# Performance work log

Measured on AMD Instinct MI355X. Metric: run time of the kernel, lower is better.

## Reference

```python
import jax, jax.numpy as jnp
import numpy as np

BN_EPS = 1e-5


def _bn(x, gamma, beta):
    # BatchNorm2d in training mode: batch statistics over (B, T, V) per channel.
    mean = jnp.mean(x, axis=(0, 2, 3), keepdims=True)
    var = jnp.var(x, axis=(0, 2, 3), keepdims=True)
    inv = jax.lax.rsqrt(var + BN_EPS)
    g = gamma[None, :, None, None]
    b = beta[None, :, None, None]
    return (x - mean) * inv * g + b


def setup_inputs() -> dict:
    key = jax.random.key(0)
    ks = jax.random.split(key, 8)
    B, Cin, Cout, T, V = 32, 64, 128, 300, 25
    x = jax.random.normal(ks[0], (B, Cin, T, V), dtype=jnp.float32)
    A_hat = jax.random.uniform(ks[1], (V, V), dtype=jnp.float32) / V  # row-normalized-ish adjacency
    # spatial 1x1 conv weight/bias
    w_sp = jax.random.normal(ks[2], (Cout, Cin), dtype=jnp.float32) * (1.0 / np.sqrt(Cin))
    b_sp = jnp.zeros((Cout,), dtype=jnp.float32)
    g_sp = jnp.ones((Cout,), dtype=jnp.float32)
    be_sp = jnp.zeros((Cout,), dtype=jnp.float32)
    # temporal conv (9,1) weight/bias, same channels
    w_t = jax.random.normal(ks[3], (Cout, Cout, 9, 1), dtype=jnp.float32) * (1.0 / np.sqrt(Cout * 9))
    b_t = jnp.zeros((Cout,), dtype=jnp.float32)
    g_t = jnp.ones((Cout,), dtype=jnp.float32)
    be_t = jnp.zeros((Cout,), dtype=jnp.float32)
    # residual 1x1 conv + BN (in_channels != out_channels)
    w_r = jax.random.normal(ks[4], (Cout, Cin), dtype=jnp.float32) * (1.0 / np.sqrt(Cin))
    b_r = jnp.zeros((Cout,), dtype=jnp.float32)
    g_r = jnp.ones((Cout,), dtype=jnp.float32)
    be_r = jnp.zeros((Cout,), dtype=jnp.float32)
    return {
        "x": x, "A_hat": A_hat,
        "w_sp": w_sp, "b_sp": b_sp, "g_sp": g_sp, "be_sp": be_sp,
        "w_t": w_t, "b_t": b_t, "g_t": g_t, "be_t": be_t,
        "w_r": w_r, "b_r": b_r, "g_r": g_r, "be_r": be_r,
    }


def reference(x, A_hat, w_sp, b_sp, g_sp, be_sp, w_t, b_t, g_t, be_t, w_r, b_r, g_r, be_r):
    # residual branch: 1x1 conv + BN
    res = jnp.einsum('oc,bctv->botv', w_r, x) + b_r[None, :, None, None]
    res = _bn(res, g_r, be_r)
    # spatial graph conv: A_hat @ x over node dim, then 1x1 conv
    h = jnp.einsum('vw,bctw->bctv', A_hat, x)
    h = jnp.einsum('oc,bctv->botv', w_sp, h) + b_sp[None, :, None, None]
    h = jax.nn.relu(_bn(h, g_sp, be_sp))
    # temporal conv (9,1) with padding (4,0), then BN
    h = jax.lax.conv_general_dilated(
        h, w_t, window_strides=(1, 1), padding=((4, 4), (0, 0)),
        dimension_numbers=('NCHW', 'OIHW', 'NCHW'))
    h = h + b_t[None, :, None, None]
    h = _bn(h, g_t, be_t)
    return jax.nn.relu(h + res)
```

## Files before the change

### kernel.cpp

```cpp
#include <hip/hip_runtime.h>

constexpr int B    = 32;
constexpr int CIN  = 64;
constexpr int COUT = 128;
constexpr int T    = 300;
constexpr int V    = 25;
constexpr int TV   = T * V;
constexpr long long NPC   = (long long)B * TV;
constexpr long long TOTAL = (long long)B * COUT * TV;

typedef short          bf16x8 __attribute__((ext_vector_type(8)));
typedef float          f32x4  __attribute__((ext_vector_type(4)));
typedef unsigned short us8    __attribute__((ext_vector_type(8)));
typedef unsigned short us4    __attribute__((ext_vector_type(4)));

static __device__ __forceinline__ unsigned short f2bf(float f) {
  union { float f; unsigned u; } x; x.f = f;
  unsigned r = x.u + 0x7FFFu + ((x.u >> 16) & 1u);
  return (unsigned short)(r >> 16);
}
static __device__ __forceinline__ float bf2f(unsigned short u) {
  union { unsigned u; float f; } x; x.u = ((unsigned)u) << 16;
  return x.f;
}
static __device__ __forceinline__ unsigned cvtpk(float a, float b) {
  unsigned r;
  asm("v_cvt_pk_bf16_f32 %0, %1, %2" : "=v"(r) : "v"(a), "v"(b));
  return r;
}

static __device__ __forceinline__ int xoff(int pos, int c) {
  return pos * 64 + ((((c >> 3)) ^ (pos & 7)) << 3) + (c & 7);
}
static __device__ __forceinline__ int soff(int c, int pw) {
  return c * 128 + ((((pw >> 3)) ^ (c & 7)) << 3) + (pw & 7);
}

__global__ __launch_bounds__(256) void kPrep(
    const float* __restrict__ w_t, const float* __restrict__ w_r,
    const float* __restrict__ w_sp, const float* __restrict__ A_hat,
    unsigned short* __restrict__ wb2, unsigned short* __restrict__ wrs2,
    unsigned short* __restrict__ bdt)
{
  int i = blockIdx.x * 256 + threadIdx.x;
  if (i < 147456) {
    int c = i & 127, ok = i >> 7;
    int k = ok % 9, o = ok / 9;
    int idx = ((k * 16 + (c >> 3)) * 128 + o) * 8 + (c & 7);
    wb2[idx] = f2bf(w_t[(o * COUT + c) * 9 + k]);
  } else if (i < 147456 + 16384) {
    int j = i - 147456;
    int c = j & 63, row = j >> 6;
    float v = (row < COUT) ? w_r[row * CIN + c] : w_sp[(row - COUT) * CIN + c];
    wrs2[((c >> 3) * 256 + row) * 8 + (c & 7)] = f2bf(v);
  } else {
    int j = i - 147456 - 16384;
    int pv = j >> 7, pw = j & 127;
    float v = 0.f;
    if (pv < 100 && pw < 100 && (pv / 25) == (pw / 25))
      v = A_hat[(pv % 25) * 25 + (pw % 25)];
    bdt[j] = f2bf(v);
  }
}

__global__ __launch_bounds__(256, 2) void kA6(
    const float* __restrict__ x, const unsigned short* __restrict__ bdt,
    const unsigned short* __restrict__ wrs2,
    unsigned short* __restrict__ resb, unsigned short* __restrict__ h,
    float2* __restrict__ part_rs)
{
  __shared__ unsigned short xs[64 * 128];
  __shared__ unsigned short xsp[112 * 64];
  unsigned short* axsp = xs;

  const int tid  = threadIdx.x;
  const int lane = tid & 63;
  const int wave = tid >> 6;
  const int b    = blockIdx.y;
  const int p0   = blockIdx.x * 100;
  const int grp  = lane >> 4;
  const int l15  = lane & 15;

  for (int u = tid; u < 16 * 128; u += 256) {
    int pos = u & 127, c4 = u >> 7;
    int c0 = c4 * 4;
    float v0 = 0.f, v1 = 0.f, v2 = 0.f, v3 = 0.f;
    if (pos < 100) {
      const float* xp = &x[(b * CIN + c0) * TV + p0 + pos];
      v0 = xp[0]; v1 = xp[TV]; v2 = xp[2 * TV]; v3 = xp[3 * TV];
    }
    unsigned short b0 = f2bf(v0), b1 = f2bf(v1), b2 = f2bf(v2), b3 = f2bf(v3);
    xs[soff(c0,     pos)] = b0;
    xs[soff(c0 + 1, pos)] = b1;
    xs[soff(c0 + 2, pos)] = b2;
    xs[soff(c0 + 3, pos)] = b3;
    if (pos < 112) {
      us4 pk = {b0, b1, b2, b3};
      *(us4*)&xsp[xoff(pos, c0)] = pk;
    }
  }
  __syncthreads();

  bf16x8 xf[4];
#pragma unroll
  for (int ks = 0; ks < 4; ++ks)
    xf[ks] = *(const bf16x8*)&xs[soff(wave * 16 + l15, ks * 32 + grp * 8)];
  __syncthreads();

  {
    f32x4 macc[7];
#pragma unroll
    for (int ni = 0; ni < 7; ++ni) macc[ni] = (f32x4)0.f;
    const int kst[7] = {0, 0, 0, 0, 1, 2, 2};
    const int kcn[7] = {1, 2, 2, 3, 3, 2, 2};
#pragma unroll
    for (int ni = 0; ni < 7; ++ni) {
      for (int kk = 0; kk < kcn[ni]; ++kk) {
        int ks = kst[ni] + kk;
        bf16x8 gf = *(const bf16x8*)&bdt[(ni * 16 + l15) * 128 + ks * 32 + grp * 8];
        macc[ni] = __builtin_amdgcn_mfma_f32_16x16x32_bf16(xf[ks], gf, macc[ni], 0, 0, 0);
      }
    }
#pragma unroll
    for (int ni = 0; ni < 7; ++ni) {
#pragma unroll
      for (int r = 0; r < 4; ++r)
        axsp[xoff(ni * 16 + l15, wave * 16 + grp * 4 + r)] = f2bf(macc[ni][r]);
    }
  }
  __syncthreads();

  const unsigned short* bsrc = (wave < 2) ? xsp : axsp;
  f32x4 acc[4][7];
#pragma unroll
  for (int m = 0; m < 4; ++m)
#pragma unroll
    for (int n = 0; n < 7; ++n) acc[m][n] = (f32x4)0.f;

#pragma unroll
  for (int ks = 0; ks < 2; ++ks) {
    bf16x8 af[4], bfr[7];
#pragma unroll
    for (int mi = 0; mi < 4; ++mi) {
      int row = wave * 64 + mi * 16 + l15;
      af[mi] = *(const bf16x8*)&wrs2[((ks * 4 + grp) * 256 + row) * 8];
    }
#pragma unroll
    for (int ni = 0; ni < 7; ++ni)
      bfr[ni] = *(const bf16x8*)&bsrc[xoff(ni * 16 + l15, ks * 32 + grp * 8)];
#pragma unroll
    for (int mi = 0; mi < 4; ++mi)
#pragma unroll
      for (int ni = 0; ni < 7; ++ni)
        acc[mi][ni] = __builtin_amdgcn_mfma_f32_16x16x32_bf16(
            af[mi], bfr[ni], acc[mi][ni], 0, 0, 0);
  }

  if (wave < 2) {
#pragma unroll
    for (int mi = 0; mi < 4; ++mi) {
#pragma unroll
      for (int ni = 0; ni < 7; ++ni) {
        int pos = ni * 16 + l15;
        if (pos < 100) {
#pragma unroll
          for (int r = 0; r < 4; ++r) {
            int c = wave * 64 + mi * 16 + grp * 4 + r;
            resb[((long long)(b * COUT + c)) * TV + p0 + pos] = f2bf(acc[mi][ni][r]);
          }
        }
      }
    }
  } else {
#pragma unroll
    for (int mi = 0; mi < 4; ++mi) {
      int o0 = (wave - 2) * 64 + mi * 16 + grp * 4;
#pragma unroll
      for (int ni = 0; ni < 7; ++ni) {
        int pos = ni * 16 + l15;
        if (pos < 100) {
          uint2 w;
          w.x = cvtpk(acc[mi][ni][0], acc[mi][ni][1]);
          w.y = cvtpk(acc[mi][ni][2], acc[mi][ni][3]);
          *(uint2*)&h[((long long)(b * TV + p0 + pos)) * COUT + o0] = w;
        }
      }
    }
  }

  {
    float sv[16], qv[16];
#pragma unroll
    for (int mi = 0; mi < 4; ++mi)
#pragma unroll
      for (int r = 0; r < 4; ++r) {
        float s = 0.f, q = 0.f;
#pragma unroll
        for (int ni = 0; ni < 7; ++ni) {
          float v = (ni < 6 || l15 < 4) ? acc[mi][ni][r] : 0.f;
          s += v; q += v * v;
        }
        sv[mi * 4 + r] = s; qv[mi * 4 + r] = q;
      }
#pragma unroll
    for (int bm = 1; bm < 16; bm <<= 1) {
      const bool up = (l15 & bm) != 0;
#pragma unroll
      for (int i = 0; i < 16; i += 2 * bm) {
        const int j = i + bm;
        float ssend = up ? sv[i] : sv[j];
        float qsend = up ? qv[i] : qv[j];
        float sgot = __shfl_xor(ssend, bm);
        float qgot = __shfl_xor(qsend, bm);
        sv[i] = (up ? sv[j] : sv[i]) + sgot;
        qv[i] = (up ? qv[j] : qv[i]) + qgot;
      }
    }
    int slot = ((l15 >> 2) * 16) + grp * 4 + (l15 & 3);
    float2* pw = &part_rs[(((long long)(blockIdx.y * 75 + blockIdx.x)) * 4 + wave) * 64];
    pw[slot] = make_float2(sv[0], qv[0]);
  }
}

__global__ __launch_bounds__(256) void kC2v2(
    const float2* __restrict__ part_rs,
    const float* __restrict__ g_r,  const float* __restrict__ be_r,
    const float* __restrict__ g_sp, const float* __restrict__ be_sp,
    float* __restrict__ scales)
{
  __shared__ float rs[256], rq[256];
  const int row = blockIdx.x;
  const int wave = row >> 6, local = row & 63;
  const int tid = threadIdx.x;
  float s = 0.f, q = 0.f;
  for (int bid = tid; bid < 2400; bid += 256) {
    float2 v = part_rs[((long long)bid * 4 + wave) * 64 + local];
    s += v.x; q += v.y;
  }
  rs[tid] = s; rq[tid] = q;
  __syncthreads();
  for (int st = 128; st > 0; st >>= 1) {
    if (tid < st) { rs[tid] += rs[tid + st]; rq[tid] += rq[tid + st]; }
    __syncthreads();
  }
  if (tid == 0) {
    const float n = (float)NPC;
    float m = rs[0] / n, var = rq[0] / n - m * m;
    float iv = rsqrtf(var + 1e-5f);
    if (row < 128) {
      float sc = g_r[row] * iv;
      scales[row] = sc; scales[128 + row] = be_r[row] - m * sc;
    } else {
      int c = row - 128;
      float sc = g_sp[c] * iv;
      scales[256 + c] = sc; scales[384 + c] = be_sp[c] - m * sc;
    }
  }
}

constexpr int NP    = 256;
constexpr int HALO  = 100;
constexpr int STAGE = NP + 2 * HALO;

__global__ __launch_bounds__(512, 2) void kE7d(
    const unsigned short* __restrict__ h, const unsigned short* __restrict__ wb2,
    const float* __restrict__ scales, unsigned short* __restrict__ cvb,
    float2* __restrict__ part_t)
{
  __shared__ unsigned short hs[STAGE * 64];
  const int tid  = threadIdx.x;
  const int lane = tid & 63;
  const int wave = tid >> 6;
  const int wm   = wave >> 2, wn = wave & 3;
  const int b    = blockIdx.y;
  const int p0   = blockIdx.x * NP;
  const int grp  = lane >> 4;
  const int l15  = lane & 15;
  const int slot = tid & 7;

  f32x4 acc[4][4];
#pragma unroll
  for (int m = 0; m < 4; ++m)
#pragma unroll
    for (int n = 0; n < 4; ++n) acc[m][n] = (f32x4)0.f;

  for (int cc = 0; cc < 2; ++cc) {
    if (cc) __syncthreads();
    const int c0 = cc * 64;
    float sc[8], sh[8];
#pragma unroll
    for (int e = 0; e < 8; ++e) {
      sc[e] = scales[256 + c0 + slot * 8 + e];
      sh[e] = scales[384 + c0 + slot * 8 + e];
    }
    for (int i = tid; i < STAGE * 8; i += 512) {
      int pos = i >> 3;
      int pg = p0 - HALO + pos;
      uint4 w = {0u, 0u, 0u, 0u};
      if (pg >= 0 && pg < TV) {
        us8 v = *(const us8*)&h[((long long)b * TV + pg) * COUT + c0 + slot * 8];
        float f[8];
#pragma unroll
        for (int e = 0; e < 8; ++e)
          f[e] = fmaxf(bf2f(v[e]) * sc[e] + sh[e], 0.f);
        w.x = cvtpk(f[0], f[1]);
        w.y = cvtpk(f[2], f[3]);
        w.z = cvtpk(f[4], f[5]);
        w.w = cvtpk(f[6], f[7]);
      }
      int si = (pos << 6) + ((slot ^ (pos & 7)) << 3);
      *(uint4*)&hs[si] = w;
    }
    __syncthreads();

    __builtin_amdgcn_s_setprio(1);
    for (int k = 0; k < 9; ++k) {
      const int plb = HALO + wn * 64 + 25 * (k - 4) + l15;
#pragma unroll
      for (int ks = 0; ks < 2; ++ks) {
        bf16x8 af[4], bfr[4];
#pragma unroll
        for (int mi = 0; mi < 4; ++mi) {
          int o = wm * 64 + mi * 16 + l15;
          af[mi] = *(const bf16x8*)&wb2[((k * 16 + cc * 8 + ks * 4 + grp) * 128 + o) * 8];
        }
#pragma unroll
        for (int ni = 0; ni < 4; ++ni) {
          int pl = plb + ni * 16;
          int si = (pl << 6) + (((ks * 4 + grp) ^ (pl & 7)) << 3);
          bfr[ni] = *(const bf16x8*)&hs[si];
        }
#pragma unroll
        for (int mi = 0; mi < 4; ++mi)
#pragma unroll
          for (int ni = 0; ni < 4; ++ni)
            acc[mi][ni] = __builtin_amdgcn_mfma_f32_16x16x32_bf16(
                af[mi], bfr[ni], acc[mi][ni], 0, 0, 0);
      }
    }
    __builtin_amdgcn_s_setprio(0);
  }

#pragma unroll
  for (int mi = 0; mi < 4; ++mi) {
#pragma unroll
    for (int ni = 0; ni < 4; ++ni) {
      int pos = p0 + wn * 64 + ni * 16 + l15;
      if (pos < TV) {
#pragma unroll
        for (int r = 0; r < 4; ++r) {
          int o = wm * 64 + mi * 16 + grp * 4 + r;
          cvb[((long long)(b * COUT + o)) * TV + pos] = f2bf(acc[mi][ni][r]);
        }
      }
    }
  }

  {
    float sv[16], qv[16];
#pragma unroll
    for (int mi = 0; mi < 4; ++mi)
#pragma unroll
      for (int r = 0; r < 4; ++r) {
        float s = 0.f, q = 0.f;
#pragma unroll
        for (int ni = 0; ni < 4; ++ni) {
          int pos = p0 + wn * 64 + ni * 16 + l15;
          float v = (pos < TV) ? acc[mi][ni][r] : 0.f;
          s += v; q += v * v;
        }
        sv[mi * 4 + r] = s; qv[mi * 4 + r] = q;
      }
#pragma unroll
    for (int bm = 1; bm < 16; bm <<= 1) {
      const bool up = (l15 & bm) != 0;
#pragma unroll
      for (int i = 0; i < 16; i += 2 * bm) {
        const int j = i + bm;
        float ssend = up ? sv[i] : sv[j];
        float qsend = up ? qv[i] : qv[j];
        float sgot = __shfl_xor(ssend, bm);
        float qgot = __shfl_xor(qsend, bm);
        sv[i] = (up ? sv[j] : sv[i]) + sgot;
        qv[i] = (up ? qv[j] : qv[i]) + qgot;
      }
    }
    int slt = ((l15 >> 2) * 16) + grp * 4 + (l15 & 3);
    float2* pw = &part_t[(((long long)(blockIdx.y * 30 + blockIdx.x)) * 8 + wave) * 64];
    pw[slt] = make_float2(sv[0], qv[0]);
  }
}

__global__ __launch_bounds__(256) void kG2(
    const float2* __restrict__ part_t,
    const float* __restrict__ g_t, const float* __restrict__ be_t,
    float* __restrict__ scales)
{
  __shared__ float rs[256], rq[256];
  const int c = blockIdx.x;
  const int wm = c >> 6, local = c & 63;
  const int tid = threadIdx.x;
  const int NB = 30 * 32;
  float s = 0.f, q = 0.f;
  for (int p = tid; p < NB * 4; p += 256) {
    int bid = p >> 2, wn = p & 3;
    float2 v = part_t[((long long)bid * 8 + (wm * 4 + wn)) * 64 + local];
    s += v.x; q += v.y;
  }
  rs[tid] = s; rq[tid] = q;
  __syncthreads();
  for (int st = 128; st > 0; st >>= 1) {
    if (tid < st) { rs[tid] += rs[tid + st]; rq[tid] += rq[tid + st]; }
    __syncthreads();
  }
  if (tid == 0) {
    const float n = (float)NPC;
    float m = rs[0] / n, var = rq[0] / n - m * m;
    float sc = g_t[c] * rsqrtf(var + 1e-5f);
    scales[512 + c] = sc;
    scales[640 + c] = be_t[c] - m * sc;
  }
}

__global__ __launch_bounds__(256) void kH(
    const unsigned short* __restrict__ cvb, const unsigned short* __restrict__ resb,
    const float* __restrict__ scales, float* __restrict__ out)
{
  const int plane = blockIdx.x;
  const int c = plane & 127;
  const float sct = scales[512 + c], sht = scales[640 + c];
  const float scr = scales[c],       shr = scales[128 + c];
  const us4* cp = (const us4*)&cvb[(long long)plane * TV];
  const us4* rp = (const us4*)&resb[(long long)plane * TV];
  float* op = &out[(long long)plane * TV];
  for (int u = threadIdx.x; u < 1875; u += 256) {
    us4 o4 = cp[u], r4 = rp[u];
    float4 y;
    y.x = fmaxf(bf2f(o4[0]) * sct + sht + bf2f(r4[0]) * scr + shr, 0.f);
    y.y = fmaxf(bf2f(o4[1]) * sct + sht + bf2f(r4[1]) * scr + shr, 0.f);
    y.z = fmaxf(bf2f(o4[2]) * sct + sht + bf2f(r4[2]) * scr + shr, 0.f);
    y.w = fmaxf(bf2f(o4[3]) * sct + sht + bf2f(r4[3]) * scr + shr, 0.f);
    *(float4*)&op[u * 4] = y;
  }
}

extern "C" void kernel_launch(void* const* d_in, const int* in_sizes, int n_in,
                              void* d_out, int out_size, void* d_ws, size_t ws_size,
                              hipStream_t stream) {
  const float* x     = (const float*)d_in[0];
  const float* A_hat = (const float*)d_in[1];
  const float* w_sp  = (const float*)d_in[2];
  const float* g_sp  = (const float*)d_in[4];
  const float* be_sp = (const float*)d_in[5];
  const float* w_t   = (const float*)d_in[6];
  const float* g_t   = (const float*)d_in[8];
  const float* be_t  = (const float*)d_in[9];
  const float* w_r   = (const float*)d_in[10];
  const float* g_r   = (const float*)d_in[12];
  const float* be_r  = (const float*)d_in[13];
  float* out = (float*)d_out;

  unsigned short* base_us = (unsigned short*)d_ws;
  unsigned short* resb = base_us;
  unsigned short* h    = base_us + (size_t)TOTAL;
  unsigned short* cvb  = base_us + (size_t)(2 * TOTAL);
  unsigned short* wb2  = base_us + (size_t)(3 * TOTAL);
  unsigned short* wrs2 = wb2 + 147456;
  unsigned short* bdt  = wrs2 + 16384;
  float2* part_rs = (float2*)(bdt + 14336);
  float2* part_t  = part_rs + 2400 * 4 * 64;
  float*  scales  = (float*)(part_t + 960 * 8 * 64);

  kPrep<<<696, 256, 0, stream>>>(w_t, w_r, w_sp, A_hat, wb2, wrs2, bdt);
  kA6<<<dim3(75, 32), 256, 0, stream>>>(x, bdt, wrs2, resb, h, part_rs);
  kC2v2<<<256, 256, 0, stream>>>(part_rs, g_r, be_r, g_sp, be_sp, scales);
  kE7d<<<dim3(30, 32), 512, 0, stream>>>(h, wb2, scales, cvb, part_t);
  kG2<<<128, 256, 0, stream>>>(part_t, g_t, be_t, scales);
  kH<<<4096, 256, 0, stream>>>(cvb, resb, scales, out);
}
```

Baseline: 235.2 us.

## Split residual and spatial branches of first kernel across grid z dimension

The first fused kernel is split over a new grid z dimension: z=0 blocks compute only the residual 1x1 conv, and z=1 blocks compute the adjacency multiply followed by the spatial 1x1 conv. Each block now handles 128 output rows instead of 256. This halves per-block registers and shared memory (single buffer), allowing a higher occupancy bound and twice as many blocks. In exchange, x is loaded and converted twice, the partial-stat layout changes, and the reduction kernel indexing is adjusted to match.

Result: faster. 227.3 us (median of 2 runs) (-3.4%).

```diff
diff --git a/kernel.cpp b/kernel.cpp
--- a/kernel.cpp
+++ b/kernel.cpp
@@ -63,109 +63,123 @@
   }
 }
 
-__global__ __launch_bounds__(256, 2) void kA6(
+__global__ __launch_bounds__(256, 3) void kA8(
     const float* __restrict__ x, const unsigned short* __restrict__ bdt,
     const unsigned short* __restrict__ wrs2,
     unsigned short* __restrict__ resb, unsigned short* __restrict__ h,
     float2* __restrict__ part_rs)
 {
-  __shared__ unsigned short xs[64 * 128];
-  __shared__ unsigned short xsp[112 * 64];
-  unsigned short* axsp = xs;
+  __shared__ unsigned short buf[64 * 128];
 
   const int tid  = threadIdx.x;
   const int lane = tid & 63;
   const int wave = tid >> 6;
   const int b    = blockIdx.y;
   const int p0   = blockIdx.x * 100;
+  const int z    = blockIdx.z;
   const int grp  = lane >> 4;
   const int l15  = lane & 15;
 
-  for (int u = tid; u < 16 * 128; u += 256) {
-    int pos = u & 127, c4 = u >> 7;
-    int c0 = c4 * 4;
-    float v0 = 0.f, v1 = 0.f, v2 = 0.f, v3 = 0.f;
-    if (pos < 100) {
-      const float* xp = &x[(b * CIN + c0) * TV + p0 + pos];
-      v0 = xp[0]; v1 = xp[TV]; v2 = xp[2 * TV]; v3 = xp[3 * TV];
-    }
-    unsigned short b0 = f2bf(v0), b1 = f2bf(v1), b2 = f2bf(v2), b3 = f2bf(v3);
-    xs[soff(c0,     pos)] = b0;
-    xs[soff(c0 + 1, pos)] = b1;
-    xs[soff(c0 + 2, pos)] = b2;
-    xs[soff(c0 + 3, pos)] = b3;
-    if (pos < 112) {
-      us4 pk = {b0, b1, b2, b3};
-      *(us4*)&xsp[xoff(pos, c0)] = pk;
-    }
-  }
-  __syncthreads();
-
-  bf16x8 xf[4];
-#pragma unroll
-  for (int ks = 0; ks < 4; ++ks)
-    xf[ks] = *(const bf16x8*)&xs[soff(wave * 16 + l15, ks * 32 + grp * 8)];
-  __syncthreads();
-
-  {
-    f32x4 macc[7];
-#pragma unroll
-    for (int ni = 0; ni < 7; ++ni) macc[ni] = (f32x4)0.f;
-    const int kst[7] = {0, 0, 0, 0, 1, 2, 2};
-    const int kcn[7] = {1, 2, 2, 3, 3, 2, 2};
-#pragma unroll
-    for (int ni = 0; ni < 7; ++ni) {
-      for (int kk = 0; kk < kcn[ni]; ++kk) {
-        int ks = kst[ni] + kk;
-        bf16x8 gf = *(const bf16x8*)&bdt[(ni * 16 + l15) * 128 + ks * 32 + grp * 8];
-        macc[ni] = __builtin_amdgcn_mfma_f32_16x16x32_bf16(xf[ks], gf, macc[ni], 0, 0, 0);
-      }
-    }
-#pragma unroll
-    for (int ni = 0; ni < 7; ++ni) {
-#pragma unroll
-      for (int r = 0; r < 4; ++r)
-        axsp[xoff(ni * 16 + l15, wave * 16 + grp * 4 + r)] = f2bf(macc[ni][r]);
-    }
-  }
-  __syncthreads();
-
-  const unsigned short* bsrc = (wave < 2) ? xsp : axsp;
-  f32x4 acc[4][7];
-#pragma unroll
-  for (int m = 0; m < 4; ++m)
+  f32x4 acc[2][7];
+#pragma unroll
+  for (int m = 0; m < 2; ++m)
 #pragma unroll
     for (int n = 0; n < 7; ++n) acc[m][n] = (f32x4)0.f;
 
+  const unsigned short* bsrc = buf;
+
+  if (z == 0) {
+    for (int u = tid; u < 16 * 112; u += 256) {
+      int pos = u % 112, c4 = u / 112;
+      int c0 = c4 * 4;
+      float v0 = 0.f, v1 = 0.f, v2 = 0.f, v3 = 0.f;
+      if (pos < 100) {
+        const float* xp = &x[(b * CIN + c0) * TV + p0 + pos];
+        v0 = xp[0]; v1 = xp[TV]; v2 = xp[2 * TV]; v3 = xp[3 * TV];
+      }
+      uint2 w;
+      w.x = cvtpk(v0, v1);
+      w.y = cvtpk(v2, v3);
+      *(uint2*)&buf[xoff(pos, c0)] = w;
+    }
+    __syncthreads();
+  } else {
+    for (int u = tid; u < 16 * 128; u += 256) {
+      int pos = u & 127, c4 = u >> 7;
+      int c0 = c4 * 4;
+      float v0 = 0.f, v1 = 0.f, v2 = 0.f, v3 = 0.f;
+      if (pos < 100) {
+        const float* xp = &x[(b * CIN + c0) * TV + p0 + pos];
+        v0 = xp[0]; v1 = xp[TV]; v2 = xp[2 * TV]; v3 = xp[3 * TV];
+      }
+      unsigned u01 = cvtpk(v0, v1), u23 = cvtpk(v2, v3);
+      buf[soff(c0,     pos)] = (unsigned short)u01;
+      buf[soff(c0 + 1, pos)] = (unsigned short)(u01 >> 16);
+      buf[soff(c0 + 2, pos)] = (unsigned short)u23;
+      buf[soff(c0 + 3, pos)] = (unsigned short)(u23 >> 16);
+    }
+    __syncthreads();
+
+    bf16x8 xf[4];
+#pragma unroll
+    for (int ks = 0; ks < 4; ++ks)
+      xf[ks] = *(const bf16x8*)&buf[soff(wave * 16 + l15, ks * 32 + grp * 8)];
+    __syncthreads();
+
+    {
+      f32x4 macc[7];
+#pragma unroll
+      for (int ni = 0; ni < 7; ++ni) macc[ni] = (f32x4)0.f;
+      const int kst[7] = {0, 0, 0, 0, 1, 2, 2};
+      const int kcn[7] = {1, 2, 2, 3, 3, 2, 2};
+#pragma unroll
+      for (int ni = 0; ni < 7; ++ni) {
+        for (int kk = 0; kk < kcn[ni]; ++kk) {
+          int ks = kst[ni] + kk;
+          bf16x8 gf = *(const bf16x8*)&bdt[(ni * 16 + l15) * 128 + ks * 32 + grp * 8];
+          macc[ni] = __builtin_amdgcn_mfma_f32_16x16x32_bf16(xf[ks], gf, macc[ni], 0, 0, 0);
+        }
+      }
+      unsigned short* axsp = (unsigned short*)buf;
+#pragma unroll
+      for (int ni = 0; ni < 7; ++ni) {
+#pragma unroll
+        for (int r = 0; r < 4; ++r)
+          axsp[xoff(ni * 16 + l15, wave * 16 + grp * 4 + r)] = f2bf(macc[ni][r]);
+      }
+    }
+    __syncthreads();
+  }
+
 #pragma unroll
   for (int ks = 0; ks < 2; ++ks) {
-    bf16x8 af[4], bfr[7];
-#pragma unroll
-    for (int mi = 0; mi < 4; ++mi) {
-      int row = wave * 64 + mi * 16 + l15;
+    bf16x8 af[2], bfr[7];
+#pragma unroll
+    for (int mi = 0; mi < 2; ++mi) {
+      int row = z * 128 + wave * 32 + mi * 16 + l15;
       af[mi] = *(const bf16x8*)&wrs2[((ks * 4 + grp) * 256 + row) * 8];
     }
 #pragma unroll
     for (int ni = 0; ni < 7; ++ni)
       bfr[ni] = *(const bf16x8*)&bsrc[xoff(ni * 16 + l15, ks * 32 + grp * 8)];
 #pragma unroll
-    for (int mi = 0; mi < 4; ++mi)
+    for (int mi = 0; mi < 2; ++mi)
 #pragma unroll
       for (int ni = 0; ni < 7; ++ni)
         acc[mi][ni] = __builtin_amdgcn_mfma_f32_16x16x32_bf16(
             af[mi], bfr[ni], acc[mi][ni], 0, 0, 0);
   }
 
-  if (wave < 2) {
-#pragma unroll
-    for (int mi = 0; mi < 4; ++mi) {
+  if (z == 0) {
+#pragma unroll
+    for (int mi = 0; mi < 2; ++mi) {
 #pragma unroll
       for (int ni = 0; ni < 7; ++ni) {
         int pos = ni * 16 + l15;
         if (pos < 100) {
 #pragma unroll
           for (int r = 0; r < 4; ++r) {
-            int c = wave * 64 + mi * 16 + grp * 4 + r;
+            int c = wave * 32 + mi * 16 + grp * 4 + r;
             resb[((long long)(b * COUT + c)) * TV + p0 + pos] = f2bf(acc[mi][ni][r]);
           }
         }
@@ -173,8 +187,8 @@
     }
   } else {
 #pragma unroll
-    for (int mi = 0; mi < 4; ++mi) {
-      int o0 = (wave - 2) * 64 + mi * 16 + grp * 4;
+    for (int mi = 0; mi < 2; ++mi) {
+      int o0 = wave * 32 + mi * 16 + grp * 4;
 #pragma unroll
       for (int ni = 0; ni < 7; ++ni) {
         int pos = ni * 16 + l15;
@@ -189,9 +203,9 @@
   }
 
   {
-    float sv[16], qv[16];
-#pragma unroll
-    for (int mi = 0; mi < 4; ++mi)
+    float sv[8], qv[8];
+#pragma unroll
+    for (int mi = 0; mi < 2; ++mi)
 #pragma unroll
       for (int r = 0; r < 4; ++r) {
         float s = 0.f, q = 0.f;
@@ -203,10 +217,10 @@
         sv[mi * 4 + r] = s; qv[mi * 4 + r] = q;
       }
 #pragma unroll
-    for (int bm = 1; bm < 16; bm <<= 1) {
+    for (int bm = 1; bm < 8; bm <<= 1) {
       const bool up = (l15 & bm) != 0;
 #pragma unroll
-      for (int i = 0; i < 16; i += 2 * bm) {
+      for (int i = 0; i < 8; i += 2 * bm) {
         const int j = i + bm;
         float ssend = up ? sv[i] : sv[j];
         float qsend = up ? qv[i] : qv[j];
@@ -216,9 +230,13 @@
         qv[i] = (up ? qv[j] : qv[i]) + qgot;
       }
     }
-    int slot = ((l15 >> 2) * 16) + grp * 4 + (l15 & 3);
-    float2* pw = &part_rs[(((long long)(blockIdx.y * 75 + blockIdx.x)) * 4 + wave) * 64];
-    pw[slot] = make_float2(sv[0], qv[0]);
+    sv[0] += __shfl_xor(sv[0], 8);
+    qv[0] += __shfl_xor(qv[0], 8);
+    if ((l15 & 8) == 0) {
+      int slot = ((l15 >> 2) * 16) + grp * 4 + (l15 & 3);
+      float2* pw = &part_rs[((((long long)(blockIdx.y * 75 + blockIdx.x)) * 2 + z) * 4 + wave) * 32];
+      pw[slot] = make_float2(sv[0], qv[0]);
+    }
   }
 }
 
@@ -230,11 +248,11 @@
 {
   __shared__ float rs[256], rq[256];
   const int row = blockIdx.x;
-  const int wave = row >> 6, local = row & 63;
+  const int z = row >> 7, wave = (row >> 5) & 3, slot = row & 31;
   const int tid = threadIdx.x;
   float s = 0.f, q = 0.f;
   for (int bid = tid; bid < 2400; bid += 256) {
-    float2 v = part_rs[((long long)bid * 4 + wave) * 64 + local];
+    float2 v = part_rs[(((long long)bid * 2 + z) * 4 + wave) * 32 + slot];
     s += v.x; q += v.y;
   }
   rs[tid] = s; rq[tid] = q;
@@ -468,11 +486,11 @@
   unsigned short* wrs2 = wb2 + 147456;
   unsigned short* bdt  = wrs2 + 16384;
   float2* part_rs = (float2*)(bdt + 14336);
-  float2* part_t  = part_rs + 2400 * 4 * 64;
+  float2* part_t  = part_rs + 2400 * 2 * 4 * 32;
   float*  scales  = (float*)(part_t + 960 * 8 * 64);
 
   kPrep<<<696, 256, 0, stream>>>(w_t, w_r, w_sp, A_hat, wb2, wrs2, bdt);
-  kA6<<<dim3(75, 32), 256, 0, stream>>>(x, bdt, wrs2, resb, h, part_rs);
+  kA8<<<dim3(75, 32, 2), 256, 0, stream>>>(x, bdt, wrs2, resb, h, part_rs);
   kC2v2<<<256, 256, 0, stream>>>(part_rs, g_r, be_r, g_sp, be_sp, scales);
   kE7d<<<dim3(30, 32), 512, 0, stream>>>(h, wb2, scales, cvb, part_t);
   kG2<<<128, 256, 0, stream>>>(part_t, g_t, be_t, scales);
```
